# Performance work log

Hardware: AMD Instinct MI355X
Metric: run time of the kernel (lower is better)

The kernel has to match this reference:

```python
import jax, jax.numpy as jnp
import numpy as np

B, T = 4096, 512          # batch, max seq len
V, E, H, O = 57, 20, 128, 18  # vocab, embed, hidden, classes


def setup_inputs() -> dict:
    key = jax.random.key(0)
    ks = jax.random.split(key, 9)
    x = jax.random.randint(ks[0], (B, T), 0, V)
    lens = jax.random.randint(ks[1], (B,), 1, T + 1)
    x_lengths = jnp.sort(lens)[::-1]  # pack_padded_sequence needs descending lengths
    s = 1.0 / np.sqrt(H)
    emb = jax.random.normal(ks[2], (V, E), dtype=jnp.float32)
    W_ih = jax.random.uniform(ks[3], (H, E), minval=-s, maxval=s, dtype=jnp.float32)
    W_hh = jax.random.uniform(ks[4], (H, H), minval=-s, maxval=s, dtype=jnp.float32)
    b_ih = jax.random.uniform(ks[5], (H,), minval=-s, maxval=s, dtype=jnp.float32)
    b_hh = jax.random.uniform(ks[6], (H,), minval=-s, maxval=s, dtype=jnp.float32)
    so = 1.0 / np.sqrt(H)
    W_out = jax.random.uniform(ks[7], (O, H), minval=-so, maxval=so, dtype=jnp.float32)
    b_out = jax.random.uniform(ks[8], (O,), minval=-so, maxval=so, dtype=jnp.float32)
    return {"x": x, "x_lengths": x_lengths, "emb": emb, "W_ih": W_ih,
            "W_hh": W_hh, "b_ih": b_ih, "b_hh": b_hh, "W_out": W_out, "b_out": b_out}


def reference(x, x_lengths, emb, W_ih, W_hh, b_ih, b_hh, W_out, b_out):
    xe = emb[x]                                            # [B,T,E] embedding gather
    # precompute input projection + both biases once (hoisted out of recurrence)
    xw = jnp.einsum('bte,he->bth', xe, W_ih) + b_ih + b_hh  # [B,T,H]
    valid = jnp.arange(T)[None, :] < x_lengths[:, None]     # [B,T] packed-seq mask

    def step(h, inp):
        xw_t, v_t = inp                                     # [B,H], [B]
        h_new = jnp.tanh(xw_t + h @ W_hh.T)
        # packed RNN: stop updating once past this sequence's length,
        # so the final h equals the hidden state at step len-1
        h = jnp.where(v_t[:, None], h_new, h)
        return h, None

    h0 = jnp.zeros((B, H), dtype=xw.dtype)
    hT, _ = jax.lax.scan(step, h0, (jnp.swapaxes(xw, 0, 1), valid.T))  # scan over T
    logits = jax.nn.relu(hT) @ W_out.T + b_out              # [B,O]
    return jax.nn.log_softmax(logits, axis=1)
```

## Files before the change

### kernel.cpp

```cpp
#include <hip/hip_runtime.h>
#include <math.h>

#define Bn 4096
#define Tn 512
#define Vn 57
#define En 20
#define Hn 128
#define On 18
#define ROWS 16
#define NTHR 512
#define NBLK (Bn / ROWS)
#define KC 5
#define ESTR 40
#define XSTR 513
#define HFSTR 132
#define ASCALE 2.8853900817779268f

typedef _Float16 half8  __attribute__((ext_vector_type(8)));
typedef __fp16   fp16x2 __attribute__((ext_vector_type(2)));
typedef float    floatx4 __attribute__((ext_vector_type(4)));

__device__ __forceinline__ float tanh_scaled(float z) {
    float e = __builtin_amdgcn_exp2f(z);
    float r = __builtin_amdgcn_rcpf(e + 1.0f);
    return fmaf(-2.0f, r, 1.0f);
}

__device__ __forceinline__ unsigned pk_u32(fp16x2 v) {
    union { fp16x2 h; unsigned u; } c; c.h = v; return c.u;
}

__launch_bounds__(NTHR, 2)
__global__ void rnn_mfma_kernel(const int* __restrict__ x,
                                const int* __restrict__ xlen,
                                const float* __restrict__ emb,
                                const float* __restrict__ W_ih,
                                const float* __restrict__ W_hh,
                                const float* __restrict__ b_ih,
                                const float* __restrict__ b_hh,
                                const float* __restrict__ W_out,
                                const float* __restrict__ b_out,
                                float* __restrict__ out)
{
    __shared__ __align__(16) uint4    exB[2][4][64];
    __shared__ __align__(16) _Float16 sEmb[Vn * ESTR];
    __shared__ __align__(16) float    sHf[ROWS * HFSTR];
    __shared__ int   sX[ROWS * XSTR];
    __shared__ float sLogit[ROWS][On];
    __shared__ float sMLS[ROWS];
    __shared__ float sPad[6800];

    const int tid  = threadIdx.x;
    const int blk  = blockIdx.x;
    const int row0 = blk * ROWS;

    ((volatile float*)sPad)[tid % 6800] = 0.0f;

    const int w    = tid >> 6;
    const int lane = tid & 63;
    const int n    = lane & 15;
    const int q    = lane >> 4;
    const int kcW  = w >> 1;
    const int bsel = w & 1;

    half8 Ah[KC];
    const int f = 32 * kcW + 8 * (n >> 2) + 4 * bsel + (n & 3);
    #pragma unroll
    for (int kc = 0; kc < 4; ++kc) {
        const float* p = &W_hh[f * Hn + kc * 32 + q * 8];
        #pragma unroll
        for (int i = 0; i < 8; ++i)
            Ah[kc][i] = (_Float16)(p[i] * ASCALE);
    }
    #pragma unroll
    for (int i = 0; i < 8; ++i) {
        int e = q * 8 + i;
        float v = 0.0f;
        if (e < En)       v = W_ih[f * En + e];
        else if (e == 20) v = b_ih[f] + b_hh[f];
        Ah[4][i] = (_Float16)(v * ASCALE);
    }

    for (int idx = tid; idx < Vn * 32; idx += NTHR) {
        int c = idx >> 5, j = idx & 31;
        float v = (j < En) ? emb[c * En + j] : (j == 20 ? 1.0f : 0.0f);
        sEmb[c * ESTR + j] = (_Float16)v;
    }
    for (int idx = tid * 4; idx < ROWS * Tn; idx += NTHR * 4) {
        int4 v = *(const int4*)&x[row0 * Tn + idx];
        int r = idx >> 9, t = idx & 511;
        sX[r * XSTR + t]     = v.x;
        sX[r * XSTR + t + 1] = v.y;
        sX[r * XSTR + t + 2] = v.z;
        sX[r * XSTR + t + 3] = v.w;
    }
    for (int idx = tid; idx < 2 * 4 * 64; idx += NTHR)
        ((uint4*)exB)[idx] = make_uint4(0u, 0u, 0u, 0u);
    __syncthreads();

    const int Lmax  = xlen[row0];
    const int len_n = xlen[row0 + n];

    int     idN;
    floatx4 P = {0.f, 0.f, 0.f, 0.f};
    {
        int id0 = sX[n * XSTR];
        half8 xe0 = *(const half8*)&sEmb[id0 * ESTR + 8 * q];
        P = __builtin_amdgcn_mfma_f32_16x16x32_f16(Ah[4], xe0, P, 0, 0, 0);
        idN = sX[n * XSTR + (Lmax > 1 ? 1 : 0)];
    }

    float hreg[4] = {0.f, 0.f, 0.f, 0.f};

    const int wOffH = 32 * kcW + 8 * q + 4 * bsel;

    #define RNN_STEP(BR, BW, t)                                                   \
    {                                                                             \
        half8 bf0 = *(const half8*)&exB[BR][0][lane];                             \
        half8 bf1 = *(const half8*)&exB[BR][1][lane];                             \
        half8 bf2 = *(const half8*)&exB[BR][2][lane];                             \
        half8 bf3 = *(const half8*)&exB[BR][3][lane];                             \
        floatx4 aE = P;                                                           \
        floatx4 aO = {0.f, 0.f, 0.f, 0.f};                                        \
        aE = __builtin_amdgcn_mfma_f32_16x16x32_f16(Ah[0], bf0, aE, 0, 0, 0);     \
        aO = __builtin_amdgcn_mfma_f32_16x16x32_f16(Ah[1], bf1, aO, 0, 0, 0);     \
        aE = __builtin_amdgcn_mfma_f32_16x16x32_f16(Ah[2], bf2, aE, 0, 0, 0);     \
        aO = __builtin_amdgcn_mfma_f32_16x16x32_f16(Ah[3], bf3, aO, 0, 0, 0);     \
        const bool upd = ((t) < len_n);                                           \
        _Pragma("unroll")                                                         \
        for (int i = 0; i < 4; ++i) {                                             \
            float v = tanh_scaled(aE[i] + aO[i]);                                 \
            hreg[i] = upd ? v : hreg[i];                                          \
        }                                                                         \
        uint2 pk;                                                                 \
        pk.x = pk_u32(__builtin_amdgcn_cvt_pkrtz(hreg[0], hreg[1]));              \
        pk.y = pk_u32(__builtin_amdgcn_cvt_pkrtz(hreg[2], hreg[3]));              \
        *(uint2*)((_Float16*)&exB[BW][kcW][0] + lane * 8 + 4 * bsel) = pk;        \
        half8 xeN = *(const half8*)&sEmb[idN * ESTR + 8 * q];                     \
        int tn = (t) + 2;                                                         \
        int idN2 = sX[n * XSTR + (tn < Lmax ? tn : Lmax - 1)];                    \
        floatx4 Pz = {0.f, 0.f, 0.f, 0.f};                                        \
        P = __builtin_amdgcn_mfma_f32_16x16x32_f16(Ah[4], xeN, Pz, 0, 0, 0);      \
        idN = idN2;                                                               \
        __syncthreads();                                                          \
    }

    int t = 0;
    for (; t + 2 <= Lmax; t += 2) {
        RNN_STEP(0, 1, t);
        RNN_STEP(1, 0, t + 1);
    }
    if (t < Lmax) {
        RNN_STEP(0, 1, t);
    }
    #undef RNN_STEP

    {
        float4 f0;
        f0.x = hreg[0]; f0.y = hreg[1]; f0.z = hreg[2]; f0.w = hreg[3];
        *(float4*)&sHf[n * HFSTR + wOffH] = f0;
    }
    __syncthreads();

    for (int it = tid; it < ROWS * On; it += NTHR) {
        int r = it / On, c = it % On;
        float acc = b_out[c];
        for (int k = 0; k < Hn; ++k) {
            float hv = sHf[r * HFSTR + k];
            hv = hv > 0.0f ? hv : 0.0f;
            acc = fmaf(hv, W_out[c * Hn + k], acc);
        }
        sLogit[r][c] = acc;
    }
    __syncthreads();

    if (tid < ROWS) {
        float m = -INFINITY;
        #pragma unroll
        for (int c = 0; c < On; ++c) m = fmaxf(m, sLogit[tid][c]);
        float s = 0.0f;
        #pragma unroll
        for (int c = 0; c < On; ++c) s += __expf(sLogit[tid][c] - m);
        sMLS[tid] = m + __logf(s);
    }
    __syncthreads();

    for (int it = tid; it < ROWS * On; it += NTHR) {
        int r = it / On, c = it % On;
        out[(row0 + r) * On + c] = sLogit[r][c] - sMLS[r];
    }
}

extern "C" void kernel_launch(void* const* d_in, const int* in_sizes, int n_in,
                              void* d_out, int out_size, void* d_ws, size_t ws_size,
                              hipStream_t stream) {
    const int*   x     = (const int*)d_in[0];
    const int*   xlen  = (const int*)d_in[1];
    const float* emb   = (const float*)d_in[2];
    const float* W_ih  = (const float*)d_in[3];
    const float* W_hh  = (const float*)d_in[4];
    const float* b_ih  = (const float*)d_in[5];
    const float* b_hh  = (const float*)d_in[6];
    const float* W_out = (const float*)d_in[7];
    const float* b_out = (const float*)d_in[8];
    float*       out   = (float*)d_out;

    rnn_mfma_kernel<<<NBLK, NTHR, 0, stream>>>(x, xlen, emb, W_ih, W_hh,
                                               b_ih, b_hh, W_out, b_out, out);
}
```

Before: 231.5 us.

## Split recurrence across two waves with own-half partial product precomputed

Cuts the block from 8 waves to 2. Each wave now computes 64 hidden units (four 16-row MFMA tiles) and holds the full W_hh slices in registers. Each wave folds its own freshly computed half of h into the next step's partial accumulator right after writing it, so only the other wave's half has to come from shared memory behind the barrier. This shortens the critical path per step and makes the barrier cheaper, at the cost of more MFMAs and VGPRs per wave and only one block per CU by launch bounds, which lowers occupancy.

Measured after the change: 662.4 us. +186.2%, slower.

```diff
diff --git a/kernel.cpp b/kernel.cpp
--- a/kernel.cpp
+++ b/kernel.cpp
@@ -8,10 +8,10 @@
 #define Hn 128
 #define On 18
 #define ROWS 16
-#define NTHR 512
+#define NTHR 128
 #define NBLK (Bn / ROWS)
 #define KC 5
-#define ESTR 40
+#define ESTR 66
 #define XSTR 513
 #define HFSTR 132
 #define ASCALE 2.8853900817779268f
@@ -30,7 +30,11 @@
     union { fp16x2 h; unsigned u; } c; c.h = v; return c.u;
 }
 
-__launch_bounds__(NTHR, 2)
+__device__ __forceinline__ half8 as_half8(uint4 v) {
+    union { uint4 u; half8 h; } c; c.u = v; return c.h;
+}
+
+__launch_bounds__(NTHR, 1)
 __global__ void rnn_mfma_kernel(const int* __restrict__ x,
                                 const int* __restrict__ xlen,
                                 const float* __restrict__ emb,
@@ -48,37 +52,40 @@
     __shared__ int   sX[ROWS * XSTR];
     __shared__ float sLogit[ROWS][On];
     __shared__ float sMLS[ROWS];
-    __shared__ float sPad[6800];
+    __shared__ float sPad[6200];
 
     const int tid  = threadIdx.x;
     const int blk  = blockIdx.x;
     const int row0 = blk * ROWS;
 
-    ((volatile float*)sPad)[tid % 6800] = 0.0f;
-
-    const int w    = tid >> 6;
+    ((volatile float*)sPad)[tid % 6200] = 0.0f;
+
+    const int u    = tid >> 6;
     const int lane = tid & 63;
     const int n    = lane & 15;
     const int q    = lane >> 4;
-    const int kcW  = w >> 1;
-    const int bsel = w & 1;
-
-    half8 Ah[KC];
-    const int f = 32 * kcW + 8 * (n >> 2) + 4 * bsel + (n & 3);
+    const int k0   = 2 * u,     k1 = 2 * u + 1;
+    const int o0   = 2 - 2 * u, o1 = 3 - 2 * u;
+
+    half8 Ah[4][KC];
     #pragma unroll
-    for (int kc = 0; kc < 4; ++kc) {
-        const float* p = &W_hh[f * Hn + kc * 32 + q * 8];
-        #pragma unroll
-        for (int i = 0; i < 8; ++i)
-            Ah[kc][i] = (_Float16)(p[i] * ASCALE);
-    }
-    #pragma unroll
-    for (int i = 0; i < 8; ++i) {
-        int e = q * 8 + i;
-        float v = 0.0f;
-        if (e < En)       v = W_ih[f * En + e];
-        else if (e == 20) v = b_ih[f] + b_hh[f];
-        Ah[4][i] = (_Float16)(v * ASCALE);
+    for (int tau = 0; tau < 4; ++tau) {
+        const int f = 64 * u + 32 * (tau >> 1) + 8 * (n >> 2) + 4 * (tau & 1) + (n & 3);
+        #pragma unroll
+        for (int kc = 0; kc < 4; ++kc) {
+            const float* p = &W_hh[f * Hn + kc * 32 + q * 8];
+            #pragma unroll
+            for (int i = 0; i < 8; ++i)
+                Ah[tau][kc][i] = (_Float16)(p[i] * ASCALE);
+        }
+        #pragma unroll
+        for (int i = 0; i < 8; ++i) {
+            int e = q * 8 + i;
+            float v = 0.0f;
+            if (e < En)       v = W_ih[f * En + e];
+            else if (e == 20) v = b_ih[f] + b_hh[f];
+            Ah[tau][4][i] = (_Float16)(v * ASCALE);
+        }
     }
 
     for (int idx = tid; idx < Vn * 32; idx += NTHR) {
@@ -102,47 +109,71 @@
     const int len_n = xlen[row0 + n];
 
     int     idN;
-    floatx4 P = {0.f, 0.f, 0.f, 0.f};
+    floatx4 P[4];
     {
         int id0 = sX[n * XSTR];
         half8 xe0 = *(const half8*)&sEmb[id0 * ESTR + 8 * q];
-        P = __builtin_amdgcn_mfma_f32_16x16x32_f16(Ah[4], xe0, P, 0, 0, 0);
+        #pragma unroll
+        for (int tau = 0; tau < 4; ++tau) {
+            floatx4 z = {0.f, 0.f, 0.f, 0.f};
+            P[tau] = __builtin_amdgcn_mfma_f32_16x16x32_f16(Ah[tau][4], xe0, z, 0, 0, 0);
+        }
         idN = sX[n * XSTR + (Lmax > 1 ? 1 : 0)];
     }
 
-    float hreg[4] = {0.f, 0.f, 0.f, 0.f};
-
-    const int wOffH = 32 * kcW + 8 * q + 4 * bsel;
-
-    #define RNN_STEP(BR, BW, t)                                                   \
-    {                                                                             \
-        half8 bf0 = *(const half8*)&exB[BR][0][lane];                             \
-        half8 bf1 = *(const half8*)&exB[BR][1][lane];                             \
-        half8 bf2 = *(const half8*)&exB[BR][2][lane];                             \
-        half8 bf3 = *(const half8*)&exB[BR][3][lane];                             \
-        floatx4 aE = P;                                                           \
-        floatx4 aO = {0.f, 0.f, 0.f, 0.f};                                        \
-        aE = __builtin_amdgcn_mfma_f32_16x16x32_f16(Ah[0], bf0, aE, 0, 0, 0);     \
-        aO = __builtin_amdgcn_mfma_f32_16x16x32_f16(Ah[1], bf1, aO, 0, 0, 0);     \
-        aE = __builtin_amdgcn_mfma_f32_16x16x32_f16(Ah[2], bf2, aE, 0, 0, 0);     \
-        aO = __builtin_amdgcn_mfma_f32_16x16x32_f16(Ah[3], bf3, aO, 0, 0, 0);     \
-        const bool upd = ((t) < len_n);                                           \
-        _Pragma("unroll")                                                         \
-        for (int i = 0; i < 4; ++i) {                                             \
-            float v = tanh_scaled(aE[i] + aO[i]);                                 \
-            hreg[i] = upd ? v : hreg[i];                                          \
-        }                                                                         \
-        uint2 pk;                                                                 \
-        pk.x = pk_u32(__builtin_amdgcn_cvt_pkrtz(hreg[0], hreg[1]));              \
-        pk.y = pk_u32(__builtin_amdgcn_cvt_pkrtz(hreg[2], hreg[3]));              \
-        *(uint2*)((_Float16*)&exB[BW][kcW][0] + lane * 8 + 4 * bsel) = pk;        \
-        half8 xeN = *(const half8*)&sEmb[idN * ESTR + 8 * q];                     \
-        int tn = (t) + 2;                                                         \
-        int idN2 = sX[n * XSTR + (tn < Lmax ? tn : Lmax - 1)];                    \
-        floatx4 Pz = {0.f, 0.f, 0.f, 0.f};                                        \
-        P = __builtin_amdgcn_mfma_f32_16x16x32_f16(Ah[4], xeN, Pz, 0, 0, 0);      \
-        idN = idN2;                                                               \
-        __syncthreads();                                                          \
+    float hreg[16];
+    #pragma unroll
+    for (int i = 0; i < 16; ++i) hreg[i] = 0.f;
+
+    #define RNN_STEP(BR, BW, t)                                                     \
+    {                                                                               \
+        half8 bo0 = *(const half8*)&exB[BR][o0][lane];                              \
+        half8 bo1 = *(const half8*)&exB[BR][o1][lane];                              \
+        half8 xeN = *(const half8*)&sEmb[idN * ESTR + 8 * q];                       \
+        int tn = (t) + 2;                                                           \
+        int idN2 = sX[n * XSTR + (tn < Lmax ? tn : Lmax - 1)];                      \
+        floatx4 a0 = __builtin_amdgcn_mfma_f32_16x16x32_f16(Ah[0][o0], bo0, P[0], 0,0,0); \
+        floatx4 a1 = __builtin_amdgcn_mfma_f32_16x16x32_f16(Ah[1][o0], bo0, P[1], 0,0,0); \
+        floatx4 a2 = __builtin_amdgcn_mfma_f32_16x16x32_f16(Ah[2][o0], bo0, P[2], 0,0,0); \
+        floatx4 a3 = __builtin_amdgcn_mfma_f32_16x16x32_f16(Ah[3][o0], bo0, P[3], 0,0,0); \
+        a0 = __builtin_amdgcn_mfma_f32_16x16x32_f16(Ah[0][o1], bo1, a0, 0, 0, 0);   \
+        a1 = __builtin_amdgcn_mfma_f32_16x16x32_f16(Ah[1][o1], bo1, a1, 0, 0, 0);   \
+        a2 = __builtin_amdgcn_mfma_f32_16x16x32_f16(Ah[2][o1], bo1, a2, 0, 0, 0);   \
+        a3 = __builtin_amdgcn_mfma_f32_16x16x32_f16(Ah[3][o1], bo1, a3, 0, 0, 0);   \
+        const bool upd = ((t) < len_n);                                             \
+        _Pragma("unroll")                                                           \
+        for (int i = 0; i < 4; ++i) {                                               \
+            float v0 = tanh_scaled(a0[i]);                                          \
+            float v1 = tanh_scaled(a1[i]);                                          \
+            float v2 = tanh_scaled(a2[i]);                                          \
+            float v3 = tanh_scaled(a3[i]);                                          \
+            hreg[i]      = upd ? v0 : hreg[i];                                      \
+            hreg[4 + i]  = upd ? v1 : hreg[4 + i];                                  \
+            hreg[8 + i]  = upd ? v2 : hreg[8 + i];                                  \
+            hreg[12 + i] = upd ? v3 : hreg[12 + i];                                 \
+        }                                                                           \
+        uint4 w0, w1;                                                               \
+        w0.x = pk_u32(__builtin_amdgcn_cvt_pkrtz(hreg[0],  hreg[1]));               \
+        w0.y = pk_u32(__builtin_amdgcn_cvt_pkrtz(hreg[2],  hreg[3]));               \
+        w0.z = pk_u32(__builtin_amdgcn_cvt_pkrtz(hreg[4],  hreg[5]));               \
+        w0.w = pk_u32(__builtin_amdgcn_cvt_pkrtz(hreg[6],  hreg[7]));               \
+        w1.x = pk_u32(__builtin_amdgcn_cvt_pkrtz(hreg[8],  hreg[9]));               \
+        w1.y = pk_u32(__builtin_amdgcn_cvt_pkrtz(hreg[10], hreg[11]));              \
+        w1.z = pk_u32(__builtin_amdgcn_cvt_pkrtz(hreg[12], hreg[13]));              \
+        w1.w = pk_u32(__builtin_amdgcn_cvt_pkrtz(hreg[14], hreg[15]));              \
+        exB[BW][k0][lane] = w0;                                                     \
+        exB[BW][k1][lane] = w1;                                                     \
+        half8 own0 = as_half8(w0);                                                  \
+        half8 own1 = as_half8(w1);                                                  \
+        _Pragma("unroll")                                                           \
+        for (int tau = 0; tau < 4; ++tau) {                                         \
+            floatx4 z = {0.f, 0.f, 0.f, 0.f};                                       \
+            P[tau] = __builtin_amdgcn_mfma_f32_16x16x32_f16(Ah[tau][4], xeN, z, 0,0,0); \
+            P[tau] = __builtin_amdgcn_mfma_f32_16x16x32_f16(Ah[tau][k0], own0, P[tau], 0,0,0); \
+            P[tau] = __builtin_amdgcn_mfma_f32_16x16x32_f16(Ah[tau][k1], own1, P[tau], 0,0,0); \
+        }                                                                           \
+        idN = idN2;                                                                 \
+        __syncthreads();                                                            \
     }
 
     int t = 0;
@@ -157,8 +188,14 @@
 
     {
         float4 f0;
-        f0.x = hreg[0]; f0.y = hreg[1]; f0.z = hreg[2]; f0.w = hreg[3];
-        *(float4*)&sHf[n * HFSTR + wOffH] = f0;
+        f0.x = hreg[0];  f0.y = hreg[1];  f0.z = hreg[2];  f0.w = hreg[3];
+        *(float4*)&sHf[n * HFSTR + 64 * u + 8 * q] = f0;
+        f0.x = hreg[4];  f0.y = hreg[5];  f0.z = hreg[6];  f0.w = hreg[7];
+        *(float4*)&sHf[n * HFSTR + 64 * u + 8 * q + 4] = f0;
+        f0.x = hreg[8];  f0.y = hreg[9];  f0.z = hreg[10]; f0.w = hreg[11];
+        *(float4*)&sHf[n * HFSTR + 64 * u + 32 + 8 * q] = f0;
+        f0.x = hreg[12]; f0.y = hreg[13]; f0.z = hreg[14]; f0.w = hreg[15];
+        *(float4*)&sHf[n * HFSTR + 64 * u + 32 + 8 * q + 4] = f0;
     }
     __syncthreads();
 
```

## Precompute embedding-times-W_ih table and reuse own hidden slice from registers

Applied to the files above, without the earlier changes.

Builds a per-block fp32 table of emb·W_ih^T plus biases for all 57 tokens and reads the input projection directly from it. This removes the per-step input MFMA, and token ids are now stored as bytes in shared memory. Each wave reorders its K-chunks so its own chunk comes first and half of it comes from registers. That cuts one shared-memory read per step, and the fp32 table lookup keeps the input term at higher precision. The cost is a larger per-block setup: 57×128 dot products of length 20, and the shared-memory padding is resized.

Result: slower. 249.4 us (+7.8%).

```diff
diff --git a/kernel.cpp b/kernel.cpp
--- a/kernel.cpp
+++ b/kernel.cpp
@@ -10,9 +10,8 @@
 #define ROWS 16
 #define NTHR 512
 #define NBLK (Bn / ROWS)
-#define KC 5
-#define ESTR 40
-#define XSTR 513
+#define XWSTR 132
+#define XBSTR 516
 #define HFSTR 132
 #define ASCALE 2.8853900817779268f
 
@@ -28,6 +27,10 @@
 
 __device__ __forceinline__ unsigned pk_u32(fp16x2 v) {
     union { fp16x2 h; unsigned u; } c; c.h = v; return c.u;
+}
+
+__device__ __forceinline__ half8 as_half8(uint4 v) {
+    union { uint4 u; half8 h; } c; c.u = v; return c.h;
 }
 
 __launch_bounds__(NTHR, 2)
@@ -42,19 +45,19 @@
                                 const float* __restrict__ b_out,
                                 float* __restrict__ out)
 {
-    __shared__ __align__(16) uint4    exB[2][4][64];
-    __shared__ __align__(16) _Float16 sEmb[Vn * ESTR];
-    __shared__ __align__(16) float    sHf[ROWS * HFSTR];
-    __shared__ int   sX[ROWS * XSTR];
+    __shared__ __align__(16) uint4 exB[2][4][64];
+    __shared__ __align__(16) float sXW[Vn * XWSTR];
+    __shared__ __align__(16) float sHf[ROWS * HFSTR];
+    __shared__ __align__(16) unsigned char sXb[ROWS * XBSTR];
     __shared__ float sLogit[ROWS][On];
     __shared__ float sMLS[ROWS];
-    __shared__ float sPad[6800];
+    __shared__ float sPad[6500];
 
     const int tid  = threadIdx.x;
     const int blk  = blockIdx.x;
     const int row0 = blk * ROWS;
 
-    ((volatile float*)sPad)[tid % 6800] = 0.0f;
+    ((volatile float*)sPad)[tid % 6500] = 0.0f;
 
     const int w    = tid >> 6;
     const int lane = tid & 63;
@@ -63,36 +66,32 @@
     const int kcW  = w >> 1;
     const int bsel = w & 1;
 
-    half8 Ah[KC];
+    half8 Ah[4];
     const int f = 32 * kcW + 8 * (n >> 2) + 4 * bsel + (n & 3);
     #pragma unroll
-    for (int kc = 0; kc < 4; ++kc) {
+    for (int j = 0; j < 4; ++j) {
+        const int kc = (kcW + j) & 3;
         const float* p = &W_hh[f * Hn + kc * 32 + q * 8];
         #pragma unroll
         for (int i = 0; i < 8; ++i)
-            Ah[kc][i] = (_Float16)(p[i] * ASCALE);
-    }
-    #pragma unroll
-    for (int i = 0; i < 8; ++i) {
-        int e = q * 8 + i;
-        float v = 0.0f;
-        if (e < En)       v = W_ih[f * En + e];
-        else if (e == 20) v = b_ih[f] + b_hh[f];
-        Ah[4][i] = (_Float16)(v * ASCALE);
-    }
-
-    for (int idx = tid; idx < Vn * 32; idx += NTHR) {
-        int c = idx >> 5, j = idx & 31;
-        float v = (j < En) ? emb[c * En + j] : (j == 20 ? 1.0f : 0.0f);
-        sEmb[c * ESTR + j] = (_Float16)v;
+            Ah[j][i] = (_Float16)(p[i] * ASCALE);
+    }
+
+    for (int idx = tid; idx < Vn * Hn; idx += NTHR) {
+        int vo = idx >> 7, ff = idx & 127;
+        float acc = b_ih[ff] + b_hh[ff];
+        #pragma unroll
+        for (int e = 0; e < En; ++e)
+            acc = fmaf(emb[vo * En + e], W_ih[ff * En + e], acc);
+        sXW[vo * XWSTR + ff] = acc * ASCALE;
     }
     for (int idx = tid * 4; idx < ROWS * Tn; idx += NTHR * 4) {
         int4 v = *(const int4*)&x[row0 * Tn + idx];
         int r = idx >> 9, t = idx & 511;
-        sX[r * XSTR + t]     = v.x;
-        sX[r * XSTR + t + 1] = v.y;
-        sX[r * XSTR + t + 2] = v.z;
-        sX[r * XSTR + t + 3] = v.w;
+        uchar4 bb;
+        bb.x = (unsigned char)v.x; bb.y = (unsigned char)v.y;
+        bb.z = (unsigned char)v.z; bb.w = (unsigned char)v.w;
+        *(uchar4*)&sXb[r * XBSTR + t] = bb;
     }
     for (int idx = tid; idx < 2 * 4 * 64; idx += NTHR)
         ((uint4*)exB)[idx] = make_uint4(0u, 0u, 0u, 0u);
@@ -100,27 +99,35 @@
 
     const int Lmax  = xlen[row0];
     const int len_n = xlen[row0 + n];
-
-    int     idN;
-    floatx4 P = {0.f, 0.f, 0.f, 0.f};
+    const int wOffH = 32 * kcW + 8 * q + 4 * bsel;
+
+    int    idN;
+    float4 XWc;
     {
-        int id0 = sX[n * XSTR];
-        half8 xe0 = *(const half8*)&sEmb[id0 * ESTR + 8 * q];
-        P = __builtin_amdgcn_mfma_f32_16x16x32_f16(Ah[4], xe0, P, 0, 0, 0);
-        idN = sX[n * XSTR + (Lmax > 1 ? 1 : 0)];
-    }
-
+        int id0 = sXb[n * XBSTR];
+        XWc = *(const float4*)&sXW[id0 * XWSTR + wOffH];
+        idN = sXb[n * XBSTR + (Lmax > 1 ? 1 : 0)];
+    }
+    uint2 own = make_uint2(0u, 0u);
     float hreg[4] = {0.f, 0.f, 0.f, 0.f};
 
-    const int wOffH = 32 * kcW + 8 * q + 4 * bsel;
+    const int j1 = (kcW + 1) & 3, j2 = (kcW + 2) & 3, j3 = (kcW + 3) & 3;
 
     #define RNN_STEP(BR, BW, t)                                                   \
     {                                                                             \
-        half8 bf0 = *(const half8*)&exB[BR][0][lane];                             \
-        half8 bf1 = *(const half8*)&exB[BR][1][lane];                             \
-        half8 bf2 = *(const half8*)&exB[BR][2][lane];                             \
-        half8 bf3 = *(const half8*)&exB[BR][3][lane];                             \
-        floatx4 aE = P;                                                           \
+        uint2 sib = *(const uint2*)((const _Float16*)&exB[BR][kcW][0]             \
+                                    + lane * 8 + 4 * (1 - bsel));                 \
+        half8 bf1 = *(const half8*)&exB[BR][j1][lane];                            \
+        half8 bf2 = *(const half8*)&exB[BR][j2][lane];                            \
+        half8 bf3 = *(const half8*)&exB[BR][j3][lane];                            \
+        float4 XWn = *(const float4*)&sXW[idN * XWSTR + wOffH];                   \
+        int tn = (t) + 2;                                                         \
+        int idN2 = sXb[n * XBSTR + (tn < Lmax ? tn : Lmax - 1)];                  \
+        uint4 ko;                                                                 \
+        ko.x = bsel ? sib.x : own.x;  ko.y = bsel ? sib.y : own.y;                \
+        ko.z = bsel ? own.x : sib.x;  ko.w = bsel ? own.y : sib.y;                \
+        half8 bf0 = as_half8(ko);                                                 \
+        floatx4 aE = {XWc.x, XWc.y, XWc.z, XWc.w};                                \
         floatx4 aO = {0.f, 0.f, 0.f, 0.f};                                        \
         aE = __builtin_amdgcn_mfma_f32_16x16x32_f16(Ah[0], bf0, aE, 0, 0, 0);     \
         aO = __builtin_amdgcn_mfma_f32_16x16x32_f16(Ah[1], bf1, aO, 0, 0, 0);     \
@@ -136,12 +143,8 @@
         pk.x = pk_u32(__builtin_amdgcn_cvt_pkrtz(hreg[0], hreg[1]));              \
         pk.y = pk_u32(__builtin_amdgcn_cvt_pkrtz(hreg[2], hreg[3]));              \
         *(uint2*)((_Float16*)&exB[BW][kcW][0] + lane * 8 + 4 * bsel) = pk;        \
-        half8 xeN = *(const half8*)&sEmb[idN * ESTR + 8 * q];                     \
-        int tn = (t) + 2;                                                         \
-        int idN2 = sX[n * XSTR + (tn < Lmax ? tn : Lmax - 1)];                    \
-        floatx4 Pz = {0.f, 0.f, 0.f, 0.f};                                        \
-        P = __builtin_amdgcn_mfma_f32_16x16x32_f16(Ah[4], xeN, Pz, 0, 0, 0);      \
-        idN = idN2;                                                               \
+        own = pk;                                                                 \
+        XWc = XWn; idN = idN2;                                                    \
         __syncthreads();                                                          \
     }
 
```

## Process 32 rows per block with register-resident own slice and byte token ids

Applied to the files above, without the earlier changes.

Doubles the rows handled per block by splitting waves into two 16-row groups, each wave computing 8 hidden units per row. The wave's own hidden slice is reused from registers instead of being reloaded from LDS, and token ids are stored as bytes to shrink shared memory. This amortizes barriers and LDS traffic over more rows, but it halves the grid to 128 blocks and lengthens the per-step serial MFMA/tanh chain per wave.

Result: slower. 315.2 us (+36.2%).

```diff
diff --git a/kernel.cpp b/kernel.cpp
--- a/kernel.cpp
+++ b/kernel.cpp
@@ -7,12 +7,12 @@
 #define En 20
 #define Hn 128
 #define On 18
-#define ROWS 16
+#define ROWS 32
 #define NTHR 512
 #define NBLK (Bn / ROWS)
 #define KC 5
 #define ESTR 40
-#define XSTR 513
+#define XBSTR 516
 #define HFSTR 132
 #define ASCALE 2.8853900817779268f
 
@@ -28,6 +28,10 @@
 
 __device__ __forceinline__ unsigned pk_u32(fp16x2 v) {
     union { fp16x2 h; unsigned u; } c; c.h = v; return c.u;
+}
+
+__device__ __forceinline__ half8 as_half8(uint4 v) {
+    union { uint4 u; half8 h; } c; c.u = v; return c.h;
 }
 
 __launch_bounds__(NTHR, 2)
@@ -42,43 +46,48 @@
                                 const float* __restrict__ b_out,
                                 float* __restrict__ out)
 {
-    __shared__ __align__(16) uint4    exB[2][4][64];
+    __shared__ __align__(16) uint4 exB[2][2][4][64];
     __shared__ __align__(16) _Float16 sEmb[Vn * ESTR];
-    __shared__ __align__(16) float    sHf[ROWS * HFSTR];
-    __shared__ int   sX[ROWS * XSTR];
+    __shared__ __align__(16) float sHf[ROWS * HFSTR];
+    __shared__ __align__(16) unsigned char sXb[ROWS * XBSTR];
     __shared__ float sLogit[ROWS][On];
     __shared__ float sMLS[ROWS];
-    __shared__ float sPad[6800];
+    __shared__ float sPad[6200];
 
     const int tid  = threadIdx.x;
     const int blk  = blockIdx.x;
     const int row0 = blk * ROWS;
 
-    ((volatile float*)sPad)[tid % 6800] = 0.0f;
+    ((volatile float*)sPad)[tid % 6200] = 0.0f;
 
     const int w    = tid >> 6;
     const int lane = tid & 63;
+    const int G    = w >> 2;
+    const int g    = w & 3;
     const int n    = lane & 15;
     const int q    = lane >> 4;
-    const int kcW  = w >> 1;
-    const int bsel = w & 1;
-
-    half8 Ah[KC];
-    const int f = 32 * kcW + 8 * (n >> 2) + 4 * bsel + (n & 3);
+    const int rloc = G * 16 + n;
+
+    half8 Ah[2][KC];
     #pragma unroll
-    for (int kc = 0; kc < 4; ++kc) {
-        const float* p = &W_hh[f * Hn + kc * 32 + q * 8];
-        #pragma unroll
-        for (int i = 0; i < 8; ++i)
-            Ah[kc][i] = (_Float16)(p[i] * ASCALE);
-    }
-    #pragma unroll
-    for (int i = 0; i < 8; ++i) {
-        int e = q * 8 + i;
-        float v = 0.0f;
-        if (e < En)       v = W_ih[f * En + e];
-        else if (e == 20) v = b_ih[f] + b_hh[f];
-        Ah[4][i] = (_Float16)(v * ASCALE);
+    for (int tau = 0; tau < 2; ++tau) {
+        const int f = 32 * g + 8 * (n >> 2) + 4 * tau + (n & 3);
+        #pragma unroll
+        for (int c = 0; c < 4; ++c) {
+            const int kc = (g + c) & 3;
+            const float* p = &W_hh[f * Hn + kc * 32 + q * 8];
+            #pragma unroll
+            for (int i = 0; i < 8; ++i)
+                Ah[tau][c][i] = (_Float16)(p[i] * ASCALE);
+        }
+        #pragma unroll
+        for (int i = 0; i < 8; ++i) {
+            int e = q * 8 + i;
+            float v = 0.0f;
+            if (e < En)       v = W_ih[f * En + e];
+            else if (e == 20) v = b_ih[f] + b_hh[f];
+            Ah[tau][4][i] = (_Float16)(v * ASCALE);
+        }
     }
 
     for (int idx = tid; idx < Vn * 32; idx += NTHR) {
@@ -89,60 +98,70 @@
     for (int idx = tid * 4; idx < ROWS * Tn; idx += NTHR * 4) {
         int4 v = *(const int4*)&x[row0 * Tn + idx];
         int r = idx >> 9, t = idx & 511;
-        sX[r * XSTR + t]     = v.x;
-        sX[r * XSTR + t + 1] = v.y;
-        sX[r * XSTR + t + 2] = v.z;
-        sX[r * XSTR + t + 3] = v.w;
-    }
-    for (int idx = tid; idx < 2 * 4 * 64; idx += NTHR)
+        uchar4 bb;
+        bb.x = (unsigned char)v.x; bb.y = (unsigned char)v.y;
+        bb.z = (unsigned char)v.z; bb.w = (unsigned char)v.w;
+        *(uchar4*)&sXb[r * XBSTR + t] = bb;
+    }
+    for (int idx = tid; idx < 2 * 2 * 4 * 64; idx += NTHR)
         ((uint4*)exB)[idx] = make_uint4(0u, 0u, 0u, 0u);
     __syncthreads();
 
     const int Lmax  = xlen[row0];
-    const int len_n = xlen[row0 + n];
+    const int len_n = xlen[row0 + rloc];
 
     int     idN;
-    floatx4 P = {0.f, 0.f, 0.f, 0.f};
+    floatx4 P0 = {0.f, 0.f, 0.f, 0.f}, P1 = {0.f, 0.f, 0.f, 0.f};
     {
-        int id0 = sX[n * XSTR];
+        int id0 = sXb[rloc * XBSTR];
         half8 xe0 = *(const half8*)&sEmb[id0 * ESTR + 8 * q];
-        P = __builtin_amdgcn_mfma_f32_16x16x32_f16(Ah[4], xe0, P, 0, 0, 0);
-        idN = sX[n * XSTR + (Lmax > 1 ? 1 : 0)];
-    }
-
-    float hreg[4] = {0.f, 0.f, 0.f, 0.f};
-
-    const int wOffH = 32 * kcW + 8 * q + 4 * bsel;
-
-    #define RNN_STEP(BR, BW, t)                                                   \
-    {                                                                             \
-        half8 bf0 = *(const half8*)&exB[BR][0][lane];                             \
-        half8 bf1 = *(const half8*)&exB[BR][1][lane];                             \
-        half8 bf2 = *(const half8*)&exB[BR][2][lane];                             \
-        half8 bf3 = *(const half8*)&exB[BR][3][lane];                             \
-        floatx4 aE = P;                                                           \
-        floatx4 aO = {0.f, 0.f, 0.f, 0.f};                                        \
-        aE = __builtin_amdgcn_mfma_f32_16x16x32_f16(Ah[0], bf0, aE, 0, 0, 0);     \
-        aO = __builtin_amdgcn_mfma_f32_16x16x32_f16(Ah[1], bf1, aO, 0, 0, 0);     \
-        aE = __builtin_amdgcn_mfma_f32_16x16x32_f16(Ah[2], bf2, aE, 0, 0, 0);     \
-        aO = __builtin_amdgcn_mfma_f32_16x16x32_f16(Ah[3], bf3, aO, 0, 0, 0);     \
-        const bool upd = ((t) < len_n);                                           \
-        _Pragma("unroll")                                                         \
-        for (int i = 0; i < 4; ++i) {                                             \
-            float v = tanh_scaled(aE[i] + aO[i]);                                 \
-            hreg[i] = upd ? v : hreg[i];                                          \
-        }                                                                         \
-        uint2 pk;                                                                 \
-        pk.x = pk_u32(__builtin_amdgcn_cvt_pkrtz(hreg[0], hreg[1]));              \
-        pk.y = pk_u32(__builtin_amdgcn_cvt_pkrtz(hreg[2], hreg[3]));              \
-        *(uint2*)((_Float16*)&exB[BW][kcW][0] + lane * 8 + 4 * bsel) = pk;        \
-        half8 xeN = *(const half8*)&sEmb[idN * ESTR + 8 * q];                     \
-        int tn = (t) + 2;                                                         \
-        int idN2 = sX[n * XSTR + (tn < Lmax ? tn : Lmax - 1)];                    \
-        floatx4 Pz = {0.f, 0.f, 0.f, 0.f};                                        \
-        P = __builtin_amdgcn_mfma_f32_16x16x32_f16(Ah[4], xeN, Pz, 0, 0, 0);      \
-        idN = idN2;                                                               \
-        __syncthreads();                                                          \
+        P0 = __builtin_amdgcn_mfma_f32_16x16x32_f16(Ah[0][4], xe0, P0, 0, 0, 0);
+        P1 = __builtin_amdgcn_mfma_f32_16x16x32_f16(Ah[1][4], xe0, P1, 0, 0, 0);
+        idN = sXb[rloc * XBSTR + (Lmax > 1 ? 1 : 0)];
+    }
+
+    uint4 own = make_uint4(0u, 0u, 0u, 0u);
+    float hreg[8] = {0.f, 0.f, 0.f, 0.f, 0.f, 0.f, 0.f, 0.f};
+
+    const int j1 = (g + 1) & 3, j2 = (g + 2) & 3, j3 = (g + 3) & 3;
+
+    #define RNN_STEP(BR, BW, t)                                                     \
+    {                                                                               \
+        half8 bf1 = *(const half8*)&exB[G][BR][j1][lane];                           \
+        half8 bf2 = *(const half8*)&exB[G][BR][j2][lane];                           \
+        half8 bf3 = *(const half8*)&exB[G][BR][j3][lane];                           \
+        half8 bo  = as_half8(own);                                                  \
+        floatx4 aE0 = __builtin_amdgcn_mfma_f32_16x16x32_f16(Ah[0][0], bo, P0, 0,0,0); \
+        floatx4 aE1 = __builtin_amdgcn_mfma_f32_16x16x32_f16(Ah[1][0], bo, P1, 0,0,0); \
+        floatx4 z0 = {0.f, 0.f, 0.f, 0.f};                                          \
+        floatx4 aO0 = __builtin_amdgcn_mfma_f32_16x16x32_f16(Ah[0][1], bf1, z0, 0,0,0); \
+        floatx4 aO1 = __builtin_amdgcn_mfma_f32_16x16x32_f16(Ah[1][1], bf1, z0, 0,0,0); \
+        aE0 = __builtin_amdgcn_mfma_f32_16x16x32_f16(Ah[0][2], bf2, aE0, 0, 0, 0);  \
+        aE1 = __builtin_amdgcn_mfma_f32_16x16x32_f16(Ah[1][2], bf2, aE1, 0, 0, 0);  \
+        aO0 = __builtin_amdgcn_mfma_f32_16x16x32_f16(Ah[0][3], bf3, aO0, 0, 0, 0);  \
+        aO1 = __builtin_amdgcn_mfma_f32_16x16x32_f16(Ah[1][3], bf3, aO1, 0, 0, 0);  \
+        const bool upd = ((t) < len_n);                                             \
+        _Pragma("unroll")                                                           \
+        for (int i = 0; i < 4; ++i) {                                               \
+            float v0 = tanh_scaled(aE0[i] + aO0[i]);                                \
+            float v1 = tanh_scaled(aE1[i] + aO1[i]);                                \
+            hreg[i]     = upd ? v0 : hreg[i];                                       \
+            hreg[4 + i] = upd ? v1 : hreg[4 + i];                                   \
+        }                                                                           \
+        uint4 pk;                                                                   \
+        pk.x = pk_u32(__builtin_amdgcn_cvt_pkrtz(hreg[0], hreg[1]));                \
+        pk.y = pk_u32(__builtin_amdgcn_cvt_pkrtz(hreg[2], hreg[3]));                \
+        pk.z = pk_u32(__builtin_amdgcn_cvt_pkrtz(hreg[4], hreg[5]));                \
+        pk.w = pk_u32(__builtin_amdgcn_cvt_pkrtz(hreg[6], hreg[7]));                \
+        exB[G][BW][g][lane] = pk;                                                   \
+        own = pk;                                                                   \
+        half8 xeN = *(const half8*)&sEmb[idN * ESTR + 8 * q];                       \
+        int tn = (t) + 2;                                                           \
+        int idN2 = sXb[rloc * XBSTR + (tn < Lmax ? tn : Lmax - 1)];                 \
+        P0 = __builtin_amdgcn_mfma_f32_16x16x32_f16(Ah[0][4], xeN, z0, 0, 0, 0);    \
+        P1 = __builtin_amdgcn_mfma_f32_16x16x32_f16(Ah[1][4], xeN, z0, 0, 0, 0);    \
+        idN = idN2;                                                                 \
+        __syncthreads();                                                            \
     }
 
     int t = 0;
@@ -158,7 +177,9 @@
     {
         float4 f0;
         f0.x = hreg[0]; f0.y = hreg[1]; f0.z = hreg[2]; f0.w = hreg[3];
-        *(float4*)&sHf[n * HFSTR + wOffH] = f0;
+        *(float4*)&sHf[rloc * HFSTR + 32 * g + 8 * q] = f0;
+        f0.x = hreg[4]; f0.y = hreg[5]; f0.z = hreg[6]; f0.w = hreg[7];
+        *(float4*)&sHf[rloc * HFSTR + 32 * g + 8 * q + 4] = f0;
     }
     __syncthreads();
 
```
